# Kernel tuning notes

Measured on AMD Instinct MI355X. Metric: run time of the kernel, lower is better.

The kernel has to match this reference:

```python
import jax, jax.numpy as jnp
import numpy as np

WINDOW = 11
C1 = 0.01 ** 2
C2 = 0.03 ** 2
PAD = WINDOW // 2


def _box_filter(img, kernel):
    # img: [B,1,H,W], kernel: [1,1,w,w]; SAME padding (odd window)
    return jax.lax.conv_general_dilated(
        img, kernel,
        window_strides=(1, 1),
        padding=[(PAD, PAD), (PAD, PAD)],
        dimension_numbers=('NCHW', 'OIHW', 'NCHW'))


def setup_inputs() -> dict:
    key = jax.random.key(0)
    kx, ky = jax.random.split(key)
    B, C, H, W = 64, 1, 512, 512
    x = jax.random.uniform(kx, (B, C, H, W), dtype=jnp.float32)
    y = jax.random.uniform(ky, (B, C, H, W), dtype=jnp.float32)
    kernel = jnp.ones((1, 1, WINDOW, WINDOW), dtype=jnp.float32) / (WINDOW ** 2)
    return {"x": x, "y": y, "kernel": kernel}


def reference(x, y, kernel):
    mu_x = _box_filter(x, kernel)
    mu_y = _box_filter(y, kernel)
    mu_x2 = mu_x * mu_x
    mu_y2 = mu_y * mu_y
    mu_xy = mu_x * mu_y
    sigma_x2 = _box_filter(x * x, kernel) - mu_x2
    sigma_y2 = _box_filter(y * y, kernel) - mu_y2
    sigma_xy = _box_filter(x * y, kernel) - mu_xy
    ssim_map = ((2.0 * mu_xy + C1) * (2.0 * sigma_xy + C2)) / (
        (mu_x2 + mu_y2 + C1) * (sigma_x2 + sigma_y2 + C2))
    return 1.0 - jnp.mean(ssim_map)
```

## Files before the change

kernel.cpp:

```cpp
#include <hip/hip_runtime.h>
#include <stdint.h>


#define IMG_H 512
#define IMG_W 512
#define N_IMG 64
#define RAD   5
#define BAND  64
#define NBANDG 8
#define NBLOCKS (N_IMG * NBANDG)
#define NSLOT 16

#define C1S2 1.4641f
#define C2S2 13.1769f

#define SLOT_BYTES 4096

typedef __attribute__((address_space(3))) uint32_t lds_u32_t;
typedef const __attribute__((address_space(1))) uint32_t glb_u32_t;

__device__ __forceinline__ void dma16(void* lds, const void* g) {
    __builtin_amdgcn_global_load_lds((glb_u32_t*)g, (lds_u32_t*)lds, 16, 0, 0);
}

__device__ __forceinline__ float dpp_shr1(float v) {
    return __int_as_float(__builtin_amdgcn_update_dpp(
        0, __float_as_int(v), 0x138, 0xF, 0xF, true));
}
__device__ __forceinline__ float dpp_shl1(float v) {
    return __int_as_float(__builtin_amdgcn_update_dpp(
        0, __float_as_int(v), 0x130, 0xF, 0xF, true));
}

__global__ __launch_bounds__(128) void ssim_fused(const float* __restrict__ x,
                                                  const float* __restrict__ y,
                                                  float* __restrict__ part)
{
    __shared__ __align__(16) char ring[NSLOT][SLOT_BYTES];

    const int tx = threadIdx.x & 63;
    const int wv = threadIdx.x >> 6;

    const int wid = (blockIdx.x & 7) * (NBLOCKS / 8) + (blockIdx.x >> 3);
    const int img = wid >> 3;
    const int bg  = wid & (NBANDG - 1);
    const int r0  = bg * BAND;
    const int q0  = r0 + wv;

    const float* __restrict__ xi = x + (size_t)img * (IMG_H * IMG_W);
    const float* __restrict__ yi = y + (size_t)img * (IMG_H * IMG_W);

    auto dma_row = [&](int slot, int ri) {
        int rc = ri < 0 ? 0 : (ri > IMG_H - 1 ? IMG_H - 1 : ri);
        char* s = &ring[slot][0];
        const char* xg = (const char*)(xi + (size_t)rc * IMG_W) + tx * 16;
        const char* yg = (const char*)(yi + (size_t)rc * IMG_W) + tx * 16;
        dma16(s,        xg);
        dma16(s + 1024, xg + 1024);
        dma16(s + 2048, yg);
        dma16(s + 3072, yg + 1024);
    };

    float Vx[8], Vy[8], Vss[8], Vxy[8];
#pragma unroll
    for (int j = 0; j < 8; ++j) { Vx[j] = 0.f; Vy[j] = 0.f; Vss[j] = 0.f; Vxy[j] = 0.f; }

    auto accum_add = [&](const char* s, float f) {
        const float4* xr = (const float4*)(s + (size_t)tx * 32);
        const float4* yr = (const float4*)(s + 2048 + (size_t)tx * 32);
        float4 x0 = xr[0], x1 = xr[1];
        float4 y0 = yr[0], y1 = yr[1];
        float xs[8] = {x0.x, x0.y, x0.z, x0.w, x1.x, x1.y, x1.z, x1.w};
        float ys[8] = {y0.x, y0.y, y0.z, y0.w, y1.x, y1.y, y1.z, y1.w};
        if (f == 1.0f) {
#pragma unroll
            for (int j = 0; j < 8; ++j) {
                Vx[j] += xs[j];
                Vy[j] += ys[j];
                Vss[j] = fmaf(xs[j], xs[j], Vss[j]);
                Vss[j] = fmaf(ys[j], ys[j], Vss[j]);
                Vxy[j] = fmaf(xs[j], ys[j], Vxy[j]);
            }
        } else {
#pragma unroll
            for (int j = 0; j < 8; ++j) {
                float fx = f * xs[j];
                float fy = f * ys[j];
                Vx[j] += fx;
                Vy[j] += fy;
                Vss[j] = fmaf(fx, xs[j], Vss[j]);
                Vss[j] = fmaf(fy, ys[j], Vss[j]);
                Vxy[j] = fmaf(fx, ys[j], Vxy[j]);
            }
        }
    };

    auto accum_sub = [&](const char* s) {
        const float4* xr = (const float4*)(s + (size_t)tx * 32);
        const float4* yr = (const float4*)(s + 2048 + (size_t)tx * 32);
        float4 x0 = xr[0], x1 = xr[1];
        float4 y0 = yr[0], y1 = yr[1];
        float xs[8] = {x0.x, x0.y, x0.z, x0.w, x1.x, x1.y, x1.z, x1.w};
        float ys[8] = {y0.x, y0.y, y0.z, y0.w, y1.x, y1.y, y1.z, y1.w};
#pragma unroll
        for (int j = 0; j < 8; ++j) {
            Vx[j]  -= xs[j];
            Vy[j]  -= ys[j];
            Vss[j] = fmaf(-xs[j], xs[j], Vss[j]);
            Vss[j] = fmaf(-ys[j], ys[j], Vss[j]);
            Vxy[j] = fmaf(-xs[j], ys[j], Vxy[j]);
        }
    };

    auto hsum = [&](const float (&V)[8], float (&S)[8]) {
        float w[18];
#pragma unroll
        for (int k = 0; k < 5; ++k) w[k] = dpp_shr1(V[3 + k]);
#pragma unroll
        for (int j = 0; j < 8; ++j) w[5 + j] = V[j];
#pragma unroll
        for (int k = 0; k < 5; ++k) w[13 + k] = dpp_shl1(V[k]);
        float s = 0.f;
#pragma unroll
        for (int t = 0; t < 11; ++t) s += w[t];
        S[0] = s;
#pragma unroll
        for (int j = 1; j < 8; ++j) { s += w[j + 10] - w[j - 1]; S[j] = s; }
    };

#pragma unroll 1
    for (int k = wv; k < 14; k += 2) dma_row(k, r0 - 7 + k);
    __syncthreads();
#pragma unroll 1
    for (int t = 0; t < 11; ++t) {
        int row = q0 - 7 + t;
        accum_add(&ring[wv + t][0], row >= 0 ? 1.0f : 0.0f);
    }

    float loss = 0.0f;
    int sa = wv + 11;
    int ss = wv;
    int sp = wv + 14;

#pragma unroll 1
    for (int i = 0; i < BAND / 2; ++i) {
        const int q = q0 + 2 * i;

        accum_add(&ring[sa][0],            (q + 4 < IMG_H) ? 1.0f : 0.0f);
        accum_add(&ring[(sa + 1) & 15][0], (q + 5 < IMG_H) ? 1.0f : 0.0f);

        if (q - 7 >= 0) accum_sub(&ring[ss][0]);
        if (q - 6 >= 0) accum_sub(&ring[(ss + 1) & 15][0]);

        if (i < BAND / 2 - 1) dma_row(sp & 15, q + 7);

        float Sx[8], Sy[8], Sss[8], Sxy[8];
        hsum(Vx,  Sx);
        hsum(Vy,  Sy);
        hsum(Vss, Sss);
        hsum(Vxy, Sxy);

#pragma unroll
        for (int j = 0; j < 8; ++j) {
            float A  = Sx[j] * Sy[j];
            float B  = fmaf(Sx[j], Sx[j], Sy[j] * Sy[j]);
            float n1 = fmaf(A, 2.0f, C1S2);
            float n2 = fmaf(Sxy[j], 242.0f, fmaf(A, -2.0f, C2S2));
            float d1 = B + C1S2;
            float d2 = fmaf(Sss[j], 121.0f, C2S2 - B);
            loss += __fdividef(n1 * n2, d1 * d2);
        }

        sa = (sa + 2) & 15;
        ss = (ss + 2) & 15;
        sp = (sp + 2) & 15;

        __syncthreads();
    }

#pragma unroll
    for (int off = 32; off > 0; off >>= 1)
        loss += __shfl_down(loss, off, 64);

    float* pr = reinterpret_cast<float*>(&ring[0][0]);
    if (tx == 0) pr[wv] = loss;
    __syncthreads();
    if (threadIdx.x == 0)
        part[blockIdx.x] = pr[0] + pr[1];
}

__global__ __launch_bounds__(256) void ssim_reduce(const float* __restrict__ part,
                                                   float* __restrict__ out)
{
    const int t  = threadIdx.x;
    const int tx = t & 63;
    float s = part[t] + part[t + 256];
#pragma unroll
    for (int off = 32; off > 0; off >>= 1)
        s += __shfl_down(s, off, 64);
    __shared__ float ws[4];
    if (tx == 0) ws[t >> 6] = s;
    __syncthreads();
    if (t == 0) {
        float total = (ws[0] + ws[1]) + (ws[2] + ws[3]);
        out[0] = 1.0f - total * (1.0f / ((float)N_IMG * IMG_H * IMG_W));
    }
}

extern "C" void kernel_launch(void* const* d_in, const int* in_sizes, int n_in,
                              void* d_out, int out_size, void* d_ws, size_t ws_size,
                              hipStream_t stream) {
    const float* x = (const float*)d_in[0];
    const float* y = (const float*)d_in[1];
    float* part = (float*)d_ws;

    ssim_fused<<<NBLOCKS, 128, 0, stream>>>(x, y, part);
    ssim_reduce<<<1, 256, 0, stream>>>(part, (float*)d_out);
}
```

Baseline: 167.9 us.

## Process four rows per barrier with padded 19-slot LDS ring

The row ring grows to 19 slots, and each slot is padded so the x and y halves avoid LDS bank conflicts, with a per-lane offset skew added for the upper half-wave. Each wave now advances two output rows per iteration, so there are four rows per __syncthreads instead of two. Two DMA rows are prefetched per iteration, and the second hsum/ssim work is interleaved to hide latency. Boundary rows are skipped by branching instead of multiplying by a 0/1 factor, and the 11-term horizontal sum is rebalanced into a tree. The cost is more LDS use and more complex slot-index wraparound.

```diff
diff --git a/kernel.cpp b/kernel.cpp
--- a/kernel.cpp
+++ b/kernel.cpp
@@ -5,16 +5,18 @@
 #define IMG_H 512
 #define IMG_W 512
 #define N_IMG 64
-#define RAD   5
 #define BAND  64
 #define NBANDG 8
 #define NBLOCKS (N_IMG * NBANDG)
-#define NSLOT 16
+#define NSLOT 19
+
+#define SLOT_BYTES 4128
+#define X1_OFF 1040
+#define Y0_OFF 2064
+#define Y1_OFF 3104
 
 #define C1S2 1.4641f
 #define C2S2 13.1769f
-
-#define SLOT_BYTES 4096
 
 typedef __attribute__((address_space(3))) uint32_t lds_u32_t;
 typedef const __attribute__((address_space(1))) uint32_t glb_u32_t;
@@ -31,6 +33,8 @@
     return __int_as_float(__builtin_amdgcn_update_dpp(
         0, __float_as_int(v), 0x130, 0xF, 0xF, true));
 }
+
+__device__ __forceinline__ int wrapS(int s) { return s >= NSLOT ? s - NSLOT : s; }
 
 __global__ __launch_bounds__(128) void ssim_fused(const float* __restrict__ x,
                                                   const float* __restrict__ y,
@@ -40,12 +44,12 @@
 
     const int tx = threadIdx.x & 63;
     const int wv = threadIdx.x >> 6;
+    const int lo = tx * 32 + ((tx & 32) >> 1);
 
     const int wid = (blockIdx.x & 7) * (NBLOCKS / 8) + (blockIdx.x >> 3);
     const int img = wid >> 3;
     const int bg  = wid & (NBANDG - 1);
     const int r0  = bg * BAND;
-    const int q0  = r0 + wv;
 
     const float* __restrict__ xi = x + (size_t)img * (IMG_H * IMG_W);
     const float* __restrict__ yi = y + (size_t)img * (IMG_H * IMG_W);
@@ -55,49 +59,36 @@
         char* s = &ring[slot][0];
         const char* xg = (const char*)(xi + (size_t)rc * IMG_W) + tx * 16;
         const char* yg = (const char*)(yi + (size_t)rc * IMG_W) + tx * 16;
-        dma16(s,        xg);
-        dma16(s + 1024, xg + 1024);
-        dma16(s + 2048, yg);
-        dma16(s + 3072, yg + 1024);
+        dma16(s,          xg);
+        dma16(s + X1_OFF, xg + 1024);
+        dma16(s + Y0_OFF, yg);
+        dma16(s + Y1_OFF, yg + 1024);
     };
 
     float Vx[8], Vy[8], Vss[8], Vxy[8];
 #pragma unroll
     for (int j = 0; j < 8; ++j) { Vx[j] = 0.f; Vy[j] = 0.f; Vss[j] = 0.f; Vxy[j] = 0.f; }
 
-    auto accum_add = [&](const char* s, float f) {
-        const float4* xr = (const float4*)(s + (size_t)tx * 32);
-        const float4* yr = (const float4*)(s + 2048 + (size_t)tx * 32);
+    auto accum_add = [&](const char* s) {
+        const float4* xr = (const float4*)(s + lo);
+        const float4* yr = (const float4*)(s + Y0_OFF + lo);
         float4 x0 = xr[0], x1 = xr[1];
         float4 y0 = yr[0], y1 = yr[1];
         float xs[8] = {x0.x, x0.y, x0.z, x0.w, x1.x, x1.y, x1.z, x1.w};
         float ys[8] = {y0.x, y0.y, y0.z, y0.w, y1.x, y1.y, y1.z, y1.w};
-        if (f == 1.0f) {
-#pragma unroll
-            for (int j = 0; j < 8; ++j) {
-                Vx[j] += xs[j];
-                Vy[j] += ys[j];
-                Vss[j] = fmaf(xs[j], xs[j], Vss[j]);
-                Vss[j] = fmaf(ys[j], ys[j], Vss[j]);
-                Vxy[j] = fmaf(xs[j], ys[j], Vxy[j]);
-            }
-        } else {
-#pragma unroll
-            for (int j = 0; j < 8; ++j) {
-                float fx = f * xs[j];
-                float fy = f * ys[j];
-                Vx[j] += fx;
-                Vy[j] += fy;
-                Vss[j] = fmaf(fx, xs[j], Vss[j]);
-                Vss[j] = fmaf(fy, ys[j], Vss[j]);
-                Vxy[j] = fmaf(fx, ys[j], Vxy[j]);
-            }
+#pragma unroll
+        for (int j = 0; j < 8; ++j) {
+            Vx[j] += xs[j];
+            Vy[j] += ys[j];
+            Vss[j] = fmaf(xs[j], xs[j], Vss[j]);
+            Vss[j] = fmaf(ys[j], ys[j], Vss[j]);
+            Vxy[j] = fmaf(xs[j], ys[j], Vxy[j]);
         }
     };
 
     auto accum_sub = [&](const char* s) {
-        const float4* xr = (const float4*)(s + (size_t)tx * 32);
-        const float4* yr = (const float4*)(s + 2048 + (size_t)tx * 32);
+        const float4* xr = (const float4*)(s + lo);
+        const float4* yr = (const float4*)(s + Y0_OFF + lo);
         float4 x0 = xr[0], x1 = xr[1];
         float4 y0 = yr[0], y1 = yr[1];
         float xs[8] = {x0.x, x0.y, x0.z, x0.w, x1.x, x1.y, x1.z, x1.w};
@@ -120,46 +111,18 @@
         for (int j = 0; j < 8; ++j) w[5 + j] = V[j];
 #pragma unroll
         for (int k = 0; k < 5; ++k) w[13 + k] = dpp_shl1(V[k]);
-        float s = 0.f;
-#pragma unroll
-        for (int t = 0; t < 11; ++t) s += w[t];
+        float s0 = (w[0] + w[1]) + (w[2] + w[3]);
+        float s1 = (w[4] + w[5]) + (w[6] + w[7]);
+        float s2 = (w[8] + w[9]) + w[10];
+        float s  = (s0 + s1) + s2;
         S[0] = s;
 #pragma unroll
         for (int j = 1; j < 8; ++j) { s += w[j + 10] - w[j - 1]; S[j] = s; }
     };
 
-#pragma unroll 1
-    for (int k = wv; k < 14; k += 2) dma_row(k, r0 - 7 + k);
-    __syncthreads();
-#pragma unroll 1
-    for (int t = 0; t < 11; ++t) {
-        int row = q0 - 7 + t;
-        accum_add(&ring[wv + t][0], row >= 0 ? 1.0f : 0.0f);
-    }
-
-    float loss = 0.0f;
-    int sa = wv + 11;
-    int ss = wv;
-    int sp = wv + 14;
-
-#pragma unroll 1
-    for (int i = 0; i < BAND / 2; ++i) {
-        const int q = q0 + 2 * i;
-
-        accum_add(&ring[sa][0],            (q + 4 < IMG_H) ? 1.0f : 0.0f);
-        accum_add(&ring[(sa + 1) & 15][0], (q + 5 < IMG_H) ? 1.0f : 0.0f);
-
-        if (q - 7 >= 0) accum_sub(&ring[ss][0]);
-        if (q - 6 >= 0) accum_sub(&ring[(ss + 1) & 15][0]);
-
-        if (i < BAND / 2 - 1) dma_row(sp & 15, q + 7);
-
-        float Sx[8], Sy[8], Sss[8], Sxy[8];
-        hsum(Vx,  Sx);
-        hsum(Vy,  Sy);
-        hsum(Vss, Sss);
-        hsum(Vxy, Sxy);
-
+    auto ssim8 = [&](const float (&Sx)[8], const float (&Sy)[8],
+                     const float (&Sss)[8], const float (&Sxy)[8],
+                     float& loss) {
 #pragma unroll
         for (int j = 0; j < 8; ++j) {
             float A  = Sx[j] * Sy[j];
@@ -170,11 +133,54 @@
             float d2 = fmaf(Sss[j], 121.0f, C2S2 - B);
             loss += __fdividef(n1 * n2, d1 * d2);
         }
-
-        sa = (sa + 2) & 15;
-        ss = (ss + 2) & 15;
-        sp = (sp + 2) & 15;
-
+    };
+
+#pragma unroll 1
+    for (int k = wv; k < 16; k += 2) dma_row(k, r0 - 7 + k);
+    __syncthreads();
+#pragma unroll 1
+    for (int t = 0; t < 11; ++t) {
+        int row = r0 + wv - 7 + t;
+        if (row >= 0) accum_add(&ring[wv + t][0]);
+    }
+
+    float loss = 0.0f;
+    int cA = 11 + wv;
+    int cS = wv;
+    int cP = 16;
+    const int po0 = 1 - wv;
+    const int po1 = 3 - wv;
+
+#pragma unroll 1
+    for (int i = 0; i < BAND / 4; ++i) {
+        const int base = r0 + 4 * i;
+        const int a = base + wv;
+
+        if (a + 4 < IMG_H) accum_add(&ring[cA][0]);
+        if (a + 5 < IMG_H) accum_add(&ring[wrapS(cA + 1)][0]);
+        if (a - 7 >= 0)    accum_sub(&ring[cS][0]);
+        if (a - 6 >= 0)    accum_sub(&ring[wrapS(cS + 1)][0]);
+
+        float Sx[8], Sy[8], Sss[8], Sxy[8];
+        hsum(Vx, Sx); hsum(Vy, Sy); hsum(Vss, Sss); hsum(Vxy, Sxy);
+
+        if (a + 6 < IMG_H) accum_add(&ring[wrapS(cA + 2)][0]);
+        if (a + 7 < IMG_H) accum_add(&ring[wrapS(cA + 3)][0]);
+        if (a - 5 >= 0)    accum_sub(&ring[wrapS(cS + 2)][0]);
+        if (a - 4 >= 0)    accum_sub(&ring[wrapS(cS + 3)][0]);
+
+        if (i < BAND / 4 - 1) {
+            dma_row(wrapS(cP + po0), base + 9 + po0);
+            dma_row(wrapS(cP + po1), base + 9 + po1);
+        }
+
+        ssim8(Sx, Sy, Sss, Sxy, loss);
+
+        float Tx[8], Ty[8], Tss[8], Txy[8];
+        hsum(Vx, Tx); hsum(Vy, Ty); hsum(Vss, Tss); hsum(Vxy, Txy);
+        ssim8(Tx, Ty, Tss, Txy, loss);
+
+        cA = wrapS(cA + 4); cS = wrapS(cS + 4); cP = wrapS(cP + 4);
         __syncthreads();
     }
 
```

Result: faster. 158.2 us (-5.8%).
